# Optimization experiments

Hardware: AMD Instinct MI355X
Metric: run time of the kernel (lower is better)

## Reference

```python
import jax, jax.numpy as jnp
import numpy as np

LN_EPS = 1e-5

def _ln(x, g):
    # LayerNorm with no bias, matching torch (population variance)
    m = x.mean(-1, keepdims=True)
    v = x.var(-1, keepdims=True)
    return (x - m) / jnp.sqrt(v + LN_EPS) * g


def setup_inputs() -> dict:
    key = jax.random.key(0)
    ks = jax.random.split(key, 10)
    B, S, D, L, V = 4, 4096, 256, 6, 32000
    std = 0.02  # nn.init.normal_(std=0.02)
    tokens = jax.random.randint(ks[0], (B, S), 0, V)
    wte = jax.random.normal(ks[1], (V, D), jnp.float32) * std
    wpe = jax.random.normal(ks[2], (S + 1, D), jnp.float32) * std  # context_size+1 table
    g_e = jnp.ones((D,), jnp.float32)
    g_p = jnp.ones((D,), jnp.float32)
    g_out = jnp.ones((D,), jnp.float32)
    ff_w1 = jax.random.normal(ks[3], (D, 4 * D), jnp.float32) * std
    ff_w2 = jax.random.normal(ks[4], (4 * D, D), jnp.float32) * std
    Wq = jax.random.normal(ks[5], (L, D, D), jnp.float32) * std
    Wk = jax.random.normal(ks[6], (L, D, D), jnp.float32) * std
    Wv = jax.random.normal(ks[7], (L, D, D), jnp.float32) * std
    return {"tokens": tokens, "wte": wte, "wpe": wpe, "g_e": g_e, "g_p": g_p,
            "g_out": g_out, "ff_w1": ff_w1, "ff_w2": ff_w2,
            "Wq": Wq, "Wk": Wk, "Wv": Wv}


def reference(tokens, wte, wpe, g_e, g_p, g_out, ff_w1, ff_w2, Wq, Wk, Wv):
    B, S = tokens.shape
    D = wte.shape[1]
    L = Wq.shape[0]
    # embeddings + pre-LN (dropout = identity at eval)
    e = _ln(wte[tokens], g_e)                 # [B,S,D] token stream
    p = _ln(wpe[:S], g_p)                     # [S,D]   positional stream (batch-invariant)
    x = e + p[None]                           # [B,S,D]
    # covariate FF on positional stream (use_ppe=True): p = p + W2 @ gelu(W1 @ p)
    p = p + jax.nn.gelu(p @ ff_w1, approximate=False) @ ff_w2
    causal = jnp.tril(jnp.ones((S, S), bool))
    inv_sqrt_d = D ** -0.5
    for l in range(L):
        # use_ppe: Q=K from positional stream (batch-invariant), V from token embeds
        q = p @ Wq[l]                          # [S,D]
        k = p @ Wk[l]                          # [S,D]
        v = jnp.einsum('bsd,de->bse', e, Wv[l])  # [B,S,D]
        s = (q @ k.T) * inv_sqrt_d             # [S,S], shared across batch
        s = jnp.where(causal, s, -jnp.inf)
        a = jax.nn.softmax(s, axis=-1)
        x = x + jnp.einsum('st,btd->bsd', a, v)
    # targets=None path: last position only
    x = x[:, -1:, :]                           # [B,1,D]
    x = _ln(x, g_out)                          # use_ln_out
    logits = x @ _ln(wte, g_e).T               # tied output head through ln_e
    return logits                              # [B,1,V]
```

## Files before the change

### kernel.cpp

```cpp
#include <hip/hip_runtime.h>
#include <hip/hip_bf16.h>

#define LN_EPS 1e-5f

typedef __attribute__((ext_vector_type(8))) short s8v;
typedef __attribute__((ext_vector_type(4))) float f32x4;

__device__ __forceinline__ float wred_sum(float v) {
#pragma unroll
  for (int o = 32; o > 0; o >>= 1) v += __shfl_xor(v, o, 64);
  return v;
}
__device__ __forceinline__ float wred_max(float v) {
#pragma unroll
  for (int o = 32; o > 0; o >>= 1) v = fmaxf(v, __shfl_xor(v, o, 64));
  return v;
}
__device__ __forceinline__ float bsum256(float v, float* s4) {
  v = wred_sum(v);
  int lane = threadIdx.x & 63, w = threadIdx.x >> 6;
  __syncthreads();
  if (lane == 0) s4[w] = v;
  __syncthreads();
  return s4[0] + s4[1] + s4[2] + s4[3];
}
__device__ __forceinline__ float bf2f(unsigned short u) {
  union { unsigned int i; float f; } c;
  c.i = ((unsigned int)u) << 16;
  return c.f;
}
__device__ __forceinline__ unsigned short f2bf(float f) {
  __hip_bfloat16 h = (__hip_bfloat16)f;
  return *(unsigned short*)&h;
}
__device__ __forceinline__ float4 bf4(ushort4 u) {
  return (float4){bf2f(u.x), bf2f(u.y), bf2f(u.z), bf2f(u.w)};
}
__device__ __forceinline__ void async_cp16(const __hip_bfloat16* g, __hip_bfloat16* l) {
  __builtin_amdgcn_global_load_lds(
      (const __attribute__((address_space(1))) unsigned int*)g,
      (__attribute__((address_space(3))) unsigned int*)l, 16, 0, 0);
}

__global__ void prep_k(const float* __restrict__ wpe, const float* __restrict__ wte,
                       const int* __restrict__ tokens,
                       const float* __restrict__ g_p, const float* __restrict__ g_e,
                       const float* __restrict__ ff_w1,
                       unsigned short* __restrict__ p0b, unsigned short* __restrict__ e,
                       unsigned short* __restrict__ w1T, float* __restrict__ zeros) {
  __shared__ float lds[64][65];
  int bx = blockIdx.x, t = threadIdx.x;
  int w = t >> 6, lane = t & 63;

  if (bx < 5120) {
    int row;
    const float* g;
    const float4* src;
    if (bx < 1024) {
      row = bx * 4 + w;
      src = (const float4*)(wpe + (size_t)row * 256);
      g = g_p;
    } else {
      row = (bx - 1024) * 4 + w;
      int tok = tokens[row];
      src = (const float4*)(wte + (size_t)tok * 256);
      g = g_e;
    }
    float4 v = src[lane];
    float mean = wred_sum(v.x + v.y + v.z + v.w) * (1.f / 256.f);
    float4 d = {v.x - mean, v.y - mean, v.z - mean, v.w - mean};
    float var = wred_sum(d.x * d.x + d.y * d.y + d.z * d.z + d.w * d.w) * (1.f / 256.f);
    float r = rsqrtf(var + LN_EPS);
    float4 gv = ((const float4*)g)[lane];
    ushort4 ob = {f2bf(d.x * r * gv.x), f2bf(d.y * r * gv.y),
                  f2bf(d.z * r * gv.z), f2bf(d.w * r * gv.w)};
    if (bx < 1024) ((ushort4*)(p0b + (size_t)row * 256))[lane] = ob;
    else           ((ushort4*)(e   + (size_t)row * 256))[lane] = ob;
    return;
  }
  if (bx < 5184) {
    int i = bx - 5120;
    int bxx = i & 3, byy = i >> 2;
    int x = t & 63, y4 = t >> 6;
    int r0 = bxx * 64, c0 = byy * 64;
#pragma unroll
    for (int k = 0; k < 16; ++k) {
      int r = y4 * 16 + k;
      lds[r][x] = ff_w1[(size_t)(r0 + r) * 1024 + c0 + x];
    }
    __syncthreads();
#pragma unroll
    for (int k = 0; k < 16; ++k) {
      int a = y4 * 16 + k;
      w1T[(size_t)(c0 + a) * 256 + r0 + x] = f2bf(lds[x][a]);
    }
    return;
  }
  for (int i = t; i < 8960; i += 256) zeros[i] = 0.f;
}

template <int TM>
__global__ __launch_bounds__(256, 4) void mfma_gemm(
    const __hip_bfloat16* __restrict__ A, const __hip_bfloat16* __restrict__ BT,
    __hip_bfloat16* __restrict__ Cout, int M, int N, int K, int mode) {
  constexpr int BM = TM * 32;
  __shared__ __hip_bfloat16 As[BM * 64];
  __shared__ __hip_bfloat16 Bs[64 * 64];
  const int t = threadIdx.x;
  const int lane = t & 63, wave = t >> 6;
  const int wr = wave >> 1, wc = wave & 1;
  const int fr = lane & 15, quad = lane >> 4;
  const int m0 = blockIdx.x * BM, n0 = blockIdx.y * 64;

  f32x4 acc[TM][2];
#pragma unroll
  for (int i = 0; i < TM; ++i)
#pragma unroll
    for (int j = 0; j < 2; ++j) acc[i][j] = (f32x4){0.f, 0.f, 0.f, 0.f};

  for (int k0 = 0; k0 < K; k0 += 64) {
    __syncthreads();
#pragma unroll
    for (int j = 0; j < TM; ++j) {
      int ld = wave * TM + j;
      int slot = ld * 64 + lane;
      int m = slot >> 3, c = slot & 7;
      const __hip_bfloat16* g = A + (size_t)(m0 + m) * K + k0 + ((c ^ (m & 7)) << 3);
      async_cp16(g, As + ld * 512);
    }
#pragma unroll
    for (int j = 0; j < 2; ++j) {
      int ld = wave * 2 + j;
      int slot = ld * 64 + lane;
      int n = slot >> 3, c = slot & 7;
      const __hip_bfloat16* g = BT + (size_t)(n0 + n) * K + k0 + ((c ^ (n & 7)) << 3);
      async_cp16(g, Bs + ld * 512);
    }
    __syncthreads();
#pragma unroll
    for (int h = 0; h < 2; ++h) {
      s8v af[TM], bfv[2];
#pragma unroll
      for (int i = 0; i < TM; ++i) {
        int m = wr * TM * 16 + i * 16 + fr;
        int ch = (h * 4 + quad) ^ (m & 7);
        af[i] = *(const s8v*)(As + m * 64 + ch * 8);
      }
#pragma unroll
      for (int j = 0; j < 2; ++j) {
        int n = wc * 32 + j * 16 + fr;
        int ch = (h * 4 + quad) ^ (n & 7);
        bfv[j] = *(const s8v*)(Bs + n * 64 + ch * 8);
      }
#pragma unroll
      for (int i = 0; i < TM; ++i)
#pragma unroll
        for (int j = 0; j < 2; ++j)
          acc[i][j] = __builtin_amdgcn_mfma_f32_16x16x32_bf16(af[i], bfv[j], acc[i][j], 0, 0, 0);
    }
  }

#pragma unroll
  for (int i = 0; i < TM; ++i) {
#pragma unroll
    for (int j = 0; j < 2; ++j) {
#pragma unroll
      for (int r = 0; r < 4; ++r) {
        int row = m0 + wr * TM * 16 + i * 16 + quad * 4 + r;
        int col = n0 + wc * 32 + j * 16 + fr;
        float v = acc[i][j][r];
        if (mode == 1) v = 0.5f * v * (1.f + erff(v * 0.70710678118654752f));
        Cout[(size_t)row * N + col] = (__hip_bfloat16)v;
      }
    }
  }
}

__global__ void plast_k(const unsigned short* __restrict__ hB,
                        const unsigned short* __restrict__ p0b,
                        const float* __restrict__ W2, float* __restrict__ plast) {
  int c = blockIdx.x, t = threadIdx.x;
  float pa = (c == 0) ? bf2f(p0b[(size_t)4095 * 256 + t]) : 0.f;
#pragma unroll
  for (int i = 0; i < 16; ++i) {
    int k = c * 16 + i;
    pa += bf2f(hB[(size_t)4095 * 1024 + k]) * W2[(size_t)k * 256 + t];
  }
  atomicAdd(&plast[t], pa);
}

__global__ void q_k(const float* __restrict__ plast, const float* __restrict__ Wq,
                    float* __restrict__ qall) {
  int c = blockIdx.x, l = blockIdx.y, t = threadIdx.x;
  const float* W = Wq + (size_t)l * 65536;
  float pa = 0.f;
#pragma unroll
  for (int i = 0; i < 16; ++i) {
    int d = c * 16 + i;
    pa += plast[d] * W[d * 256 + t];
  }
  atomicAdd(&qall[l * 256 + t], pa);
}

__global__ void kv_k(const float* __restrict__ Wk, const float* __restrict__ qall,
                     float* __restrict__ kv) {
  int l = blockIdx.y;
  int w = threadIdx.x >> 6, lane = threadIdx.x & 63;
  int r = blockIdx.x * 4 + w;
  float4 wv = ((const float4*)(Wk + (size_t)l * 65536 + (size_t)r * 256))[lane];
  float4 qv = ((const float4*)(qall + l * 256))[lane];
  float dot = wred_sum(wv.x * qv.x + wv.y * qv.y + wv.z * qv.z + wv.w * qv.w);
  if (lane == 0) kv[l * 256 + r] = dot;
}

__global__ void w2kv_k(const float* __restrict__ W2, const float* __restrict__ kv,
                       float* __restrict__ w2kv) {
  int l = blockIdx.y;
  int w = threadIdx.x >> 6, lane = threadIdx.x & 63;
  int r = blockIdx.x * 4 + w;
  float4 wv = ((const float4*)(W2 + (size_t)r * 256))[lane];
  float4 qv = ((const float4*)(kv + l * 256))[lane];
  float dot = wred_sum(wv.x * qv.x + wv.y * qv.y + wv.z * qv.z + wv.w * qv.w);
  if (lane == 0) w2kv[l * 1024 + r] = dot;
}

__global__ __launch_bounds__(256) void sc_k(
    const unsigned short* __restrict__ p0b, const unsigned short* __restrict__ hB,
    const float* __restrict__ kv, const float* __restrict__ w2kv,
    float* __restrict__ sc) {
  __shared__ float skv[6 * 256];
  __shared__ float sw2[6 * 1024];
  int t = threadIdx.x;
  for (int i = t; i < 1536; i += 256) skv[i] = kv[i];
  for (int i = t; i < 6144; i += 256) sw2[i] = w2kv[i];
  __syncthreads();
  int wave = t >> 6, lane = t & 63;
#pragma unroll
  for (int rr = 0; rr < 2; ++rr) {
    int row = blockIdx.x * 8 + wave * 2 + rr;
    const ushort4* hrow = (const ushort4*)(hB + (size_t)row * 1024);
    float4 h0 = bf4(hrow[lane]);
    float4 h1 = bf4(hrow[64 + lane]);
    float4 h2 = bf4(hrow[128 + lane]);
    float4 h3 = bf4(hrow[192 + lane]);
    float4 p = bf4(((const ushort4*)(p0b + (size_t)row * 256))[lane]);
#pragma unroll
    for (int l = 0; l < 6; ++l) {
      float4 kf = ((const float4*)(skv + l * 256))[lane];
      float4 w0 = ((const float4*)(sw2 + l * 1024))[lane];
      float4 w1 = ((const float4*)(sw2 + l * 1024 + 256))[lane];
      float4 w2 = ((const float4*)(sw2 + l * 1024 + 512))[lane];
      float4 w3 = ((const float4*)(sw2 + l * 1024 + 768))[lane];
      float a = p.x * kf.x + p.y * kf.y + p.z * kf.z + p.w * kf.w;
      a += h0.x * w0.x + h0.y * w0.y + h0.z * w0.z + h0.w * w0.w;
      a += h1.x * w1.x + h1.y * w1.y + h1.z * w1.z + h1.w * w1.w;
      a += h2.x * w2.x + h2.y * w2.y + h2.z * w2.z + h2.w * w2.w;
      a += h3.x * w3.x + h3.y * w3.y + h3.z * w3.z + h3.w * w3.w;
      a = wred_sum(a);
      if (lane == 0) sc[(size_t)l * 4096 + row] = a * 0.0625f;
    }
  }
}

__global__ void softmax_k(const float* __restrict__ sc, float* __restrict__ w) {
  int l = blockIdx.x, t = threadIdx.x;
  float4 v = ((const float4*)(sc + (size_t)l * 4096))[t];
  float m = fmaxf(fmaxf(v.x, v.y), fmaxf(v.z, v.w));
  m = wred_max(m);
  __shared__ float red[16];
  __shared__ float red2[16];
  int lane = t & 63, wv = t >> 6;
  if (lane == 0) red[wv] = m;
  __syncthreads();
  float mm = red[0];
#pragma unroll
  for (int i = 1; i < 16; ++i) mm = fmaxf(mm, red[i]);
  float e0 = expf(v.x - mm), e1 = expf(v.y - mm), e2 = expf(v.z - mm), e3 = expf(v.w - mm);
  float s = wred_sum(e0 + e1 + e2 + e3);
  if (lane == 0) red2[wv] = s;
  __syncthreads();
  float tot = 0.f;
#pragma unroll
  for (int i = 0; i < 16; ++i) tot += red2[i];
  float inv = 1.f / tot;
  float4 o = {e0 * inv, e1 * inv, e2 * inv, e3 * inv};
  ((float4*)(w + (size_t)l * 4096))[t] = o;
}

__global__ void ctx_k(const unsigned short* __restrict__ e, const float* __restrict__ w,
                      float* __restrict__ ctx) {
  int c = blockIdx.x, b = blockIdx.y, t = threadIdx.x;
  const unsigned short* eb = e + ((size_t)b * 4096 + c * 32) * 256;
  const float* w0 = w + c * 32;
  float a[6] = {0.f, 0.f, 0.f, 0.f, 0.f, 0.f};
#pragma unroll 4
  for (int i = 0; i < 32; ++i) {
    float ev = bf2f(eb[(size_t)i * 256 + t]);
#pragma unroll
    for (int l = 0; l < 6; ++l) a[l] += w0[l * 4096 + i] * ev;
  }
#pragma unroll
  for (int l = 0; l < 6; ++l) atomicAdd(&ctx[(l * 4 + b) * 256 + t], a[l]);
}

__global__ void proj_k(const float* __restrict__ ctx, const float* __restrict__ Wv,
                       float* __restrict__ xacc) {
  int c = blockIdx.x, l = blockIdx.y, t = threadIdx.x;
  const float* W = Wv + (size_t)l * 65536;
  float pa[4] = {0.f, 0.f, 0.f, 0.f};
#pragma unroll
  for (int i = 0; i < 16; ++i) {
    int d = c * 16 + i;
    float wv = W[d * 256 + t];
#pragma unroll
    for (int b = 0; b < 4; ++b) pa[b] += ctx[(l * 4 + b) * 256 + d] * wv;
  }
#pragma unroll
  for (int b = 0; b < 4; ++b) atomicAdd(&xacc[b * 256 + t], pa[b]);
}

__global__ void final_k(const unsigned short* __restrict__ e, const unsigned short* __restrict__ p0b,
                        const float* __restrict__ xacc, const float* __restrict__ gout,
                        float* __restrict__ xln) {
  int b = blockIdx.x, t = threadIdx.x;
  float v = xacc[b * 256 + t] + bf2f(e[((size_t)(b * 4096 + 4095)) * 256 + t]) +
            bf2f(p0b[(size_t)4095 * 256 + t]);
  __shared__ float s4[4];
  float mean = bsum256(v, s4) * (1.f / 256.f);
  float d = v - mean;
  float var = bsum256(d * d, s4) * (1.f / 256.f);
  xln[b * 256 + t] = d * rsqrtf(var + LN_EPS) * gout[t];
}

__global__ void logits_k(const float* __restrict__ wte, const float* __restrict__ ge,
                         const float* __restrict__ xln, float* __restrict__ out) {
  int wv = threadIdx.x >> 6, lane = threadIdx.x & 63;
  int v = blockIdx.x * 4 + wv;
  float4 x = ((const float4*)(wte + (size_t)v * 256))[lane];
  float mean = wred_sum(x.x + x.y + x.z + x.w) * (1.f / 256.f);
  float4 d = {x.x - mean, x.y - mean, x.z - mean, x.w - mean};
  float var = wred_sum(d.x * d.x + d.y * d.y + d.z * d.z + d.w * d.w) * (1.f / 256.f);
  float r = rsqrtf(var + LN_EPS);
  float4 gv = ((const float4*)ge)[lane];
  float4 ln = {d.x * r * gv.x, d.y * r * gv.y, d.z * r * gv.z, d.w * r * gv.w};
#pragma unroll
  for (int b = 0; b < 4; ++b) {
    float4 xv = ((const float4*)(xln + b * 256))[lane];
    float dot = wred_sum(ln.x * xv.x + ln.y * xv.y + ln.z * xv.z + ln.w * xv.w);
    if (lane == 0) out[b * 32000 + v] = dot;
  }
}

#define O_E     ((size_t)0)
#define O_P0B   ((size_t)2097152)
#define O_W1T   ((size_t)2621440)
#define O_HB    ((size_t)2752512)
#define O_CTX   ((size_t)4849664)
#define O_QALL  ((size_t)4855808)
#define O_XACC  ((size_t)4857344)
#define O_PLAST ((size_t)4858368)
#define O_KV    ((size_t)4858624)
#define O_W2KV  ((size_t)4860160)
#define O_SC    ((size_t)4866304)
#define O_WSM   ((size_t)4890880)
#define O_XLN   ((size_t)4915456)

extern "C" void kernel_launch(void* const* d_in, const int* in_sizes, int n_in,
                              void* d_out, int out_size, void* d_ws, size_t ws_size,
                              hipStream_t stream) {
  const int*   tokens = (const int*)d_in[0];
  const float* wte    = (const float*)d_in[1];
  const float* wpe    = (const float*)d_in[2];
  const float* g_e    = (const float*)d_in[3];
  const float* g_p    = (const float*)d_in[4];
  const float* g_out  = (const float*)d_in[5];
  const float* ff_w1  = (const float*)d_in[6];
  const float* ff_w2  = (const float*)d_in[7];
  const float* Wq     = (const float*)d_in[8];
  const float* Wk     = (const float*)d_in[9];
  const float* Wv     = (const float*)d_in[10];
  float* out = (float*)d_out;
  float* ws = (float*)d_ws;

  unsigned short* e   = (unsigned short*)(ws + O_E);
  unsigned short* p0b = (unsigned short*)(ws + O_P0B);
  unsigned short* w1T = (unsigned short*)(ws + O_W1T);
  unsigned short* hB  = (unsigned short*)(ws + O_HB);
  float* ctx   = ws + O_CTX;
  float* qall  = ws + O_QALL;
  float* xacc  = ws + O_XACC;
  float* plast = ws + O_PLAST;
  float* kv    = ws + O_KV;
  float* w2kv  = ws + O_W2KV;
  float* sc    = ws + O_SC;
  float* wsm   = ws + O_WSM;
  float* xln   = ws + O_XLN;

  prep_k<<<5185, 256, 0, stream>>>(wpe, wte, tokens, g_p, g_e, ff_w1,
                                   p0b, e, w1T, ctx);
  mfma_gemm<2><<<dim3(64, 16), 256, 0, stream>>>(
      (const __hip_bfloat16*)p0b, (const __hip_bfloat16*)w1T,
      (__hip_bfloat16*)hB, 4096, 1024, 256, 1);
  plast_k<<<64, 256, 0, stream>>>(hB, p0b, ff_w2, plast);
  q_k<<<dim3(16, 6), 256, 0, stream>>>(plast, Wq, qall);
  kv_k<<<dim3(64, 6), 256, 0, stream>>>(Wk, qall, kv);
  w2kv_k<<<dim3(256, 6), 256, 0, stream>>>(ff_w2, kv, w2kv);
  sc_k<<<512, 256, 0, stream>>>(p0b, hB, kv, w2kv, sc);
  softmax_k<<<6, 1024, 0, stream>>>(sc, wsm);
  ctx_k<<<dim3(128, 4), 256, 0, stream>>>(e, wsm, ctx);
  proj_k<<<dim3(16, 6), 256, 0, stream>>>(ctx, Wv, xacc);
  final_k<<<4, 256, 0, stream>>>(e, p0b, xacc, g_out, xln);
  logits_k<<<8000, 256, 0, stream>>>(wte, g_e, xln, out);
}
```

Measured before the change: 155.3 us.

## Fuse softmax into ctx kernel, fuse final LN into proj, widen GEMM K-tile

Removes the separate softmax kernel: each ctx block recomputes the row max and sum for all six layers from the raw scores, then normalises its own 32-weight chunk in shared memory. The final LayerNorm is folded into the projection kernel using an atomic completion counter, so the last block does the LN. The MFMA GEMM now uses 64x128 K-tiles with a 16-way swizzle instead of the templated 64-wide tile. This cuts two kernel launches and one round trip through global memory, at the cost of redundant softmax reductions in every ctx block (512 blocks each reading 6x4096 scores).

```diff
diff --git a/kernel.cpp b/kernel.cpp
--- a/kernel.cpp
+++ b/kernel.cpp
@@ -23,6 +23,14 @@
   if (lane == 0) s4[w] = v;
   __syncthreads();
   return s4[0] + s4[1] + s4[2] + s4[3];
+}
+__device__ __forceinline__ float bmax256(float v, float* s4) {
+  v = wred_max(v);
+  int lane = threadIdx.x & 63, w = threadIdx.x >> 6;
+  __syncthreads();
+  if (lane == 0) s4[w] = v;
+  __syncthreads();
+  return fmaxf(fmaxf(s4[0], s4[1]), fmaxf(s4[2], s4[3]));
 }
 __device__ __forceinline__ float bf2f(unsigned short u) {
   union { unsigned int i; float f; } c;
@@ -96,64 +104,62 @@
     }
     return;
   }
-  for (int i = t; i < 8960; i += 256) zeros[i] = 0.f;
-}
-
-template <int TM>
+  for (int i = t; i < 8976; i += 256) zeros[i] = 0.f;
+}
+
 __global__ __launch_bounds__(256, 4) void mfma_gemm(
     const __hip_bfloat16* __restrict__ A, const __hip_bfloat16* __restrict__ BT,
     __hip_bfloat16* __restrict__ Cout, int M, int N, int K, int mode) {
-  constexpr int BM = TM * 32;
-  __shared__ __hip_bfloat16 As[BM * 64];
-  __shared__ __hip_bfloat16 Bs[64 * 64];
+  __shared__ __hip_bfloat16 As[64 * 128];
+  __shared__ __hip_bfloat16 Bs[64 * 128];
   const int t = threadIdx.x;
   const int lane = t & 63, wave = t >> 6;
   const int wr = wave >> 1, wc = wave & 1;
   const int fr = lane & 15, quad = lane >> 4;
-  const int m0 = blockIdx.x * BM, n0 = blockIdx.y * 64;
-
-  f32x4 acc[TM][2];
-#pragma unroll
-  for (int i = 0; i < TM; ++i)
+  const int m0 = blockIdx.x * 64, n0 = blockIdx.y * 64;
+
+  f32x4 acc[2][2];
+#pragma unroll
+  for (int i = 0; i < 2; ++i)
 #pragma unroll
     for (int j = 0; j < 2; ++j) acc[i][j] = (f32x4){0.f, 0.f, 0.f, 0.f};
 
-  for (int k0 = 0; k0 < K; k0 += 64) {
+  for (int k0 = 0; k0 < K; k0 += 128) {
     __syncthreads();
 #pragma unroll
-    for (int j = 0; j < TM; ++j) {
-      int ld = wave * TM + j;
+    for (int j = 0; j < 4; ++j) {
+      int ld = wave * 4 + j;
       int slot = ld * 64 + lane;
-      int m = slot >> 3, c = slot & 7;
-      const __hip_bfloat16* g = A + (size_t)(m0 + m) * K + k0 + ((c ^ (m & 7)) << 3);
+      int m = slot >> 4, c = slot & 15;
+      const __hip_bfloat16* g = A + (size_t)(m0 + m) * K + k0 + ((c ^ (m & 15)) << 3);
       async_cp16(g, As + ld * 512);
     }
 #pragma unroll
-    for (int j = 0; j < 2; ++j) {
-      int ld = wave * 2 + j;
+    for (int j = 0; j < 4; ++j) {
+      int ld = wave * 4 + j;
       int slot = ld * 64 + lane;
-      int n = slot >> 3, c = slot & 7;
-      const __hip_bfloat16* g = BT + (size_t)(n0 + n) * K + k0 + ((c ^ (n & 7)) << 3);
+      int n = slot >> 4, c = slot & 15;
+      const __hip_bfloat16* g = BT + (size_t)(n0 + n) * K + k0 + ((c ^ (n & 15)) << 3);
       async_cp16(g, Bs + ld * 512);
     }
     __syncthreads();
 #pragma unroll
-    for (int h = 0; h < 2; ++h) {
-      s8v af[TM], bfv[2];
-#pragma unroll
-      for (int i = 0; i < TM; ++i) {
-        int m = wr * TM * 16 + i * 16 + fr;
-        int ch = (h * 4 + quad) ^ (m & 7);
-        af[i] = *(const s8v*)(As + m * 64 + ch * 8);
+    for (int h = 0; h < 4; ++h) {
+      s8v af[2], bfv[2];
+#pragma unroll
+      for (int i = 0; i < 2; ++i) {
+        int m = wr * 32 + i * 16 + fr;
+        int ch = (h * 4 + quad) ^ (m & 15);
+        af[i] = *(const s8v*)(As + m * 128 + ch * 8);
       }
 #pragma unroll
       for (int j = 0; j < 2; ++j) {
         int n = wc * 32 + j * 16 + fr;
-        int ch = (h * 4 + quad) ^ (n & 7);
-        bfv[j] = *(const s8v*)(Bs + n * 64 + ch * 8);
+        int ch = (h * 4 + quad) ^ (n & 15);
+        bfv[j] = *(const s8v*)(Bs + n * 128 + ch * 8);
       }
 #pragma unroll
-      for (int i = 0; i < TM; ++i)
+      for (int i = 0; i < 2; ++i)
 #pragma unroll
         for (int j = 0; j < 2; ++j)
           acc[i][j] = __builtin_amdgcn_mfma_f32_16x16x32_bf16(af[i], bfv[j], acc[i][j], 0, 0, 0);
@@ -161,12 +167,12 @@
   }
 
 #pragma unroll
-  for (int i = 0; i < TM; ++i) {
+  for (int i = 0; i < 2; ++i) {
 #pragma unroll
     for (int j = 0; j < 2; ++j) {
 #pragma unroll
       for (int r = 0; r < 4; ++r) {
-        int row = m0 + wr * TM * 16 + i * 16 + quad * 4 + r;
+        int row = m0 + wr * 32 + i * 16 + quad * 4 + r;
         int col = n0 + wc * 32 + j * 16 + fr;
         float v = acc[i][j][r];
         if (mode == 1) v = 0.5f * v * (1.f + erff(v * 0.70710678118654752f));
@@ -262,50 +268,49 @@
   }
 }
 
-__global__ void softmax_k(const float* __restrict__ sc, float* __restrict__ w) {
-  int l = blockIdx.x, t = threadIdx.x;
-  float4 v = ((const float4*)(sc + (size_t)l * 4096))[t];
-  float m = fmaxf(fmaxf(v.x, v.y), fmaxf(v.z, v.w));
-  m = wred_max(m);
-  __shared__ float red[16];
-  __shared__ float red2[16];
-  int lane = t & 63, wv = t >> 6;
-  if (lane == 0) red[wv] = m;
-  __syncthreads();
-  float mm = red[0];
-#pragma unroll
-  for (int i = 1; i < 16; ++i) mm = fmaxf(mm, red[i]);
-  float e0 = expf(v.x - mm), e1 = expf(v.y - mm), e2 = expf(v.z - mm), e3 = expf(v.w - mm);
-  float s = wred_sum(e0 + e1 + e2 + e3);
-  if (lane == 0) red2[wv] = s;
-  __syncthreads();
-  float tot = 0.f;
-#pragma unroll
-  for (int i = 0; i < 16; ++i) tot += red2[i];
-  float inv = 1.f / tot;
-  float4 o = {e0 * inv, e1 * inv, e2 * inv, e3 * inv};
-  ((float4*)(w + (size_t)l * 4096))[t] = o;
-}
-
-__global__ void ctx_k(const unsigned short* __restrict__ e, const float* __restrict__ w,
-                      float* __restrict__ ctx) {
+__global__ void ctx_sm_k(const unsigned short* __restrict__ e, const float* __restrict__ sc,
+                         float* __restrict__ ctx) {
   int c = blockIdx.x, b = blockIdx.y, t = threadIdx.x;
+  __shared__ float s4[4];
+  __shared__ float wch[6][32];
+  float wmax[6], winv[6];
+#pragma unroll
+  for (int l = 0; l < 6; ++l) {
+    const float* scl = sc + (size_t)l * 4096;
+    float lm = -1e30f;
+    for (int i = t; i < 4096; i += 256) lm = fmaxf(lm, scl[i]);
+    lm = bmax256(lm, s4);
+    float ls = 0.f;
+    for (int i = t; i < 4096; i += 256) ls += expf(scl[i] - lm);
+    ls = bsum256(ls, s4);
+    wmax[l] = lm; winv[l] = 1.f / ls;
+  }
+  if (t < 192) {
+    int l = t >> 5, j = t & 31;
+    wch[l][j] = expf(sc[(size_t)l * 4096 + c * 32 + j] - wmax[l]) * winv[l];
+  }
+  __syncthreads();
   const unsigned short* eb = e + ((size_t)b * 4096 + c * 32) * 256;
-  const float* w0 = w + c * 32;
   float a[6] = {0.f, 0.f, 0.f, 0.f, 0.f, 0.f};
 #pragma unroll 4
   for (int i = 0; i < 32; ++i) {
     float ev = bf2f(eb[(size_t)i * 256 + t]);
 #pragma unroll
-    for (int l = 0; l < 6; ++l) a[l] += w0[l * 4096 + i] * ev;
+    for (int l = 0; l < 6; ++l) a[l] += wch[l][i] * ev;
   }
 #pragma unroll
   for (int l = 0; l < 6; ++l) atomicAdd(&ctx[(l * 4 + b) * 256 + t], a[l]);
 }
 
-__global__ void proj_k(const float* __restrict__ ctx, const float* __restrict__ Wv,
-                       float* __restrict__ xacc) {
+__global__ void proj_final_k(const float* __restrict__ ctx, const float* __restrict__ Wv,
+                             float* __restrict__ xacc,
+                             const unsigned short* __restrict__ e,
+                             const unsigned short* __restrict__ p0b,
+                             const float* __restrict__ gout, float* __restrict__ xln,
+                             int* __restrict__ done) {
   int c = blockIdx.x, l = blockIdx.y, t = threadIdx.x;
+  __shared__ float s4[4];
+  __shared__ int tick;
   const float* W = Wv + (size_t)l * 65536;
   float pa[4] = {0.f, 0.f, 0.f, 0.f};
 #pragma unroll
@@ -317,19 +322,21 @@
   }
 #pragma unroll
   for (int b = 0; b < 4; ++b) atomicAdd(&xacc[b * 256 + t], pa[b]);
-}
-
-__global__ void final_k(const unsigned short* __restrict__ e, const unsigned short* __restrict__ p0b,
-                        const float* __restrict__ xacc, const float* __restrict__ gout,
-                        float* __restrict__ xln) {
-  int b = blockIdx.x, t = threadIdx.x;
-  float v = xacc[b * 256 + t] + bf2f(e[((size_t)(b * 4096 + 4095)) * 256 + t]) +
-            bf2f(p0b[(size_t)4095 * 256 + t]);
-  __shared__ float s4[4];
-  float mean = bsum256(v, s4) * (1.f / 256.f);
-  float d = v - mean;
-  float var = bsum256(d * d, s4) * (1.f / 256.f);
-  xln[b * 256 + t] = d * rsqrtf(var + LN_EPS) * gout[t];
+  __threadfence();
+  if (t == 0) tick = atomicAdd(done, 1);
+  __syncthreads();
+  if (tick == 95) {
+#pragma unroll
+    for (int b = 0; b < 4; ++b) {
+      float v = atomicAdd(&xacc[b * 256 + t], 0.f)
+              + bf2f(e[((size_t)(b * 4096 + 4095)) * 256 + t])
+              + bf2f(p0b[(size_t)4095 * 256 + t]);
+      float mean = bsum256(v, s4) * (1.f / 256.f);
+      float d = v - mean;
+      float var = bsum256(d * d, s4) * (1.f / 256.f);
+      xln[b * 256 + t] = d * rsqrtf(var + LN_EPS) * gout[t];
+    }
+  }
 }
 
 __global__ void logits_k(const float* __restrict__ wte, const float* __restrict__ ge,
@@ -359,11 +366,11 @@
 #define O_QALL  ((size_t)4855808)
 #define O_XACC  ((size_t)4857344)
 #define O_PLAST ((size_t)4858368)
-#define O_KV    ((size_t)4858624)
-#define O_W2KV  ((size_t)4860160)
-#define O_SC    ((size_t)4866304)
-#define O_WSM   ((size_t)4890880)
-#define O_XLN   ((size_t)4915456)
+#define O_DONE  ((size_t)4858624)
+#define O_KV    ((size_t)4858640)
+#define O_W2KV  ((size_t)4860176)
+#define O_SC    ((size_t)4866320)
+#define O_XLN   ((size_t)4890896)
 
 extern "C" void kernel_launch(void* const* d_in, const int* in_sizes, int n_in,
                               void* d_out, int out_size, void* d_ws, size_t ws_size,
@@ -390,15 +397,15 @@
   float* qall  = ws + O_QALL;
   float* xacc  = ws + O_XACC;
   float* plast = ws + O_PLAST;
+  int*   done  = (int*)(ws + O_DONE);
   float* kv    = ws + O_KV;
   float* w2kv  = ws + O_W2KV;
   float* sc    = ws + O_SC;
-  float* wsm   = ws + O_WSM;
   float* xln   = ws + O_XLN;
 
   prep_k<<<5185, 256, 0, stream>>>(wpe, wte, tokens, g_p, g_e, ff_w1,
                                    p0b, e, w1T, ctx);
-  mfma_gemm<2><<<dim3(64, 16), 256, 0, stream>>>(
+  mfma_gemm<<<dim3(64, 16), 256, 0, stream>>>(
       (const __hip_bfloat16*)p0b, (const __hip_bfloat16*)w1T,
       (__hip_bfloat16*)hB, 4096, 1024, 256, 1);
   plast_k<<<64, 256, 0, stream>>>(hB, p0b, ff_w2, plast);
@@ -406,9 +413,7 @@
   kv_k<<<dim3(64, 6), 256, 0, stream>>>(Wk, qall, kv);
   w2kv_k<<<dim3(256, 6), 256, 0, stream>>>(ff_w2, kv, w2kv);
   sc_k<<<512, 256, 0, stream>>>(p0b, hB, kv, w2kv, sc);
-  softmax_k<<<6, 1024, 0, stream>>>(sc, wsm);
-  ctx_k<<<dim3(128, 4), 256, 0, stream>>>(e, wsm, ctx);
-  proj_k<<<dim3(16, 6), 256, 0, stream>>>(ctx, Wv, xacc);
-  final_k<<<4, 256, 0, stream>>>(e, p0b, xacc, g_out, xln);
+  ctx_sm_k<<<dim3(128, 4), 256, 0, stream>>>(e, sc, ctx);
+  proj_final_k<<<dim3(16, 6), 256, 0, stream>>>(ctx, Wv, xacc, e, p0b, g_out, xln, done);
   logits_k<<<8000, 256, 0, stream>>>(wte, g_e, xln, out);
 }
```

Result: slower. 184.9 us (+19.1%).
